# Optimization experiments

Measured on AMD Instinct MI355X. Metric: run time of the kernel, lower is better.

## Reference

```python
import jax, jax.numpy as jnp
import numpy as np

EMBEDDING_DIM = 128
METRIC_MARGIN = 1.0
EPS = 1e-8


def setup_inputs() -> dict:
    key = jax.random.key(0)
    X = jax.random.normal(key, (8192, EMBEDDING_DIM), dtype=jnp.float32)
    return {"X": X}


def reference(X):
    B, d = X.shape
    P = B // 2  # number of positive pairs (2p, 2p+1)
    # Pairwise similarity matrix (original uses broadcasted mul+sum; this is the GEMM form)
    D = (X @ X.T) / d  # [B, B]
    E = jnp.exp(D + METRIC_MARGIN)  # [B, B]

    # For pair p: sum of exp over rows 2p and 2p+1, excluding columns {2p, 2p+1}
    pair_row_sum = E.sum(axis=1).reshape(P, 2).sum(axis=1)  # [P]
    # 2x2 diagonal blocks E[2p:2p+2, 2p:2p+2]
    blocks = jnp.einsum('pipj->pij', E.reshape(P, 2, P, 2))  # [P, 2, 2]
    S = pair_row_sum - blocks.sum(axis=(1, 2))  # [P]

    even = jnp.arange(0, B, 2)
    D_pos = D[even, even + 1]  # D[2p, 2p+1], [P]

    J = jnp.log(EPS + S) - D_pos  # [P]
    loss = jnp.mean(jnp.maximum(J, 0.0) ** 2) / 2.0
    return loss
```

## Files before the change

### kernel.cpp

```cpp
#include <hip/hip_runtime.h>
#include <hip/hip_bf16.h>

#define NROWS 8192
#define DIM   128
#define NPAIR (NROWS / 2)
#define CSPLIT 16
#define COLS_PER_CS (NROWS / CSPLIT)
#define CTILE 64
#define NT (COLS_PER_CS / CTILE)
#define MREP 2
#define ROWS_PER_BLOCK 128

typedef __attribute__((ext_vector_type(8))) short bf16x8;
typedef __attribute__((ext_vector_type(4))) float f32x4;

__device__ inline float exp2_fast(float x) {
#if __has_builtin(__builtin_amdgcn_exp2f)
    return __builtin_amdgcn_exp2f(x);
#else
    return exp2f(x);
#endif
}

__device__ inline unsigned short f2bf(float f) {
    unsigned int u = __float_as_uint(f);
    unsigned int r = (u + 0x7fffu + ((u >> 16) & 1u)) >> 16;
    return (unsigned short)r;
}

#define SCL_F 0.0112710550069450f
#define E1_F  2.7182818284590452f

__global__ __launch_bounds__(256) void k_convert(const float* __restrict__ X,
                                                 unsigned short* __restrict__ Xa,
                                                 unsigned short* __restrict__ Xc) {
    int id = blockIdx.x * 256 + threadIdx.x;
    float4 v = reinterpret_cast<const float4*>(X)[id];
    ushort4 oa, oc;
    oa.x = f2bf(v.x * SCL_F); oa.y = f2bf(v.y * SCL_F);
    oa.z = f2bf(v.z * SCL_F); oa.w = f2bf(v.w * SCL_F);
    oc.x = f2bf(v.x); oc.y = f2bf(v.y); oc.z = f2bf(v.z); oc.w = f2bf(v.w);
    reinterpret_cast<ushort4*>(Xa)[id] = oa;
    reinterpret_cast<ushort4*>(Xc)[id] = oc;
}

__global__ __launch_bounds__(256, 4) void k_rowsum(const unsigned short* __restrict__ Xa,
                                                   const unsigned short* __restrict__ Xc,
                                                   float* __restrict__ partial) {
    __shared__ unsigned short Bt[CTILE * DIM];
    const int tid  = threadIdx.x;
    const int wave = tid >> 6;
    const int lane = tid & 63;
    const int l15  = lane & 15;
    const int lhi  = lane >> 4;
    const int rowbase = blockIdx.x * ROWS_PER_BLOCK + wave * (MREP * 16);
    const int cs = blockIdx.y;

    bf16x8 a00, a01, a02, a03, a10, a11, a12, a13;
    {
        const unsigned short* r0 = Xa + (size_t)(rowbase + l15) * DIM + lhi * 8;
        const unsigned short* r1 = r0 + 16 * DIM;
        a00 = *reinterpret_cast<const bf16x8*>(r0);
        a01 = *reinterpret_cast<const bf16x8*>(r0 + 32);
        a02 = *reinterpret_cast<const bf16x8*>(r0 + 64);
        a03 = *reinterpret_cast<const bf16x8*>(r0 + 96);
        a10 = *reinterpret_cast<const bf16x8*>(r1);
        a11 = *reinterpret_cast<const bf16x8*>(r1 + 32);
        a12 = *reinterpret_cast<const bf16x8*>(r1 + 64);
        a13 = *reinterpret_cast<const bf16x8*>(r1 + 96);
    }
    asm volatile("" : "+v"(a00), "+v"(a01), "+v"(a02), "+v"(a03));
    asm volatile("" : "+v"(a10), "+v"(a11), "+v"(a12), "+v"(a13));

    f32x4 esum0 = {0.f, 0.f, 0.f, 0.f};
    f32x4 esum1 = {0.f, 0.f, 0.f, 0.f};

    const int tcol = tid >> 4;
    const int tseg = tid & 15;
    const unsigned short* gsrc = Xc + (size_t)(cs * COLS_PER_CS + tcol) * DIM + tseg * 8;
    const int lslot = (tcol << 4) | (tseg ^ (tcol & 7));

    bf16x8 st0, st1, st2, st3;
    st0 = *reinterpret_cast<const bf16x8*>(gsrc);
    st1 = *reinterpret_cast<const bf16x8*>(gsrc + 16 * DIM);
    st2 = *reinterpret_cast<const bf16x8*>(gsrc + 32 * DIM);
    st3 = *reinterpret_cast<const bf16x8*>(gsrc + 48 * DIM);

    for (int it = 0; it < NT; ++it) {
        if (it) __syncthreads();
        *reinterpret_cast<bf16x8*>(&Bt[(size_t)(lslot      ) * 8]) = st0;
        *reinterpret_cast<bf16x8*>(&Bt[(size_t)(lslot + 256) * 8]) = st1;
        *reinterpret_cast<bf16x8*>(&Bt[(size_t)(lslot + 512) * 8]) = st2;
        *reinterpret_cast<bf16x8*>(&Bt[(size_t)(lslot + 768) * 8]) = st3;
        __syncthreads();

        if (it + 1 < NT) {
            const unsigned short* nb = gsrc + (size_t)(it + 1) * CTILE * DIM;
            st0 = *reinterpret_cast<const bf16x8*>(nb);
            st1 = *reinterpret_cast<const bf16x8*>(nb + 16 * DIM);
            st2 = *reinterpret_cast<const bf16x8*>(nb + 32 * DIM);
            st3 = *reinterpret_cast<const bf16x8*>(nb + 48 * DIM);
        }

        const int x = l15 & 7;
#pragma unroll
        for (int ct = 0; ct < CTILE / 16; ++ct) {
            const unsigned short* lb = &Bt[(size_t)(ct * 16 + l15) * DIM];
            bf16x8 b0 = *reinterpret_cast<const bf16x8*>(lb + ((lhi      ^ x) * 8));
            bf16x8 b1 = *reinterpret_cast<const bf16x8*>(lb + (((lhi + 4 ) ^ x) * 8));
            bf16x8 b2 = *reinterpret_cast<const bf16x8*>(lb + (((lhi + 8 ) ^ x) * 8));
            bf16x8 b3 = *reinterpret_cast<const bf16x8*>(lb + (((lhi + 12) ^ x) * 8));

            f32x4 d0 = {0.f, 0.f, 0.f, 0.f};
            f32x4 d1 = {0.f, 0.f, 0.f, 0.f};
            d0 = __builtin_amdgcn_mfma_f32_16x16x32_bf16(a00, b0, d0, 0, 0, 0);
            d1 = __builtin_amdgcn_mfma_f32_16x16x32_bf16(a10, b0, d1, 0, 0, 0);
            d0 = __builtin_amdgcn_mfma_f32_16x16x32_bf16(a01, b1, d0, 0, 0, 0);
            d1 = __builtin_amdgcn_mfma_f32_16x16x32_bf16(a11, b1, d1, 0, 0, 0);
            d0 = __builtin_amdgcn_mfma_f32_16x16x32_bf16(a02, b2, d0, 0, 0, 0);
            d1 = __builtin_amdgcn_mfma_f32_16x16x32_bf16(a12, b2, d1, 0, 0, 0);
            d0 = __builtin_amdgcn_mfma_f32_16x16x32_bf16(a03, b3, d0, 0, 0, 0);
            d1 = __builtin_amdgcn_mfma_f32_16x16x32_bf16(a13, b3, d1, 0, 0, 0);

            esum0[0] += exp2_fast(d0[0]); esum0[1] += exp2_fast(d0[1]);
            esum0[2] += exp2_fast(d0[2]); esum0[3] += exp2_fast(d0[3]);
            esum1[0] += exp2_fast(d1[0]); esum1[1] += exp2_fast(d1[1]);
            esum1[2] += exp2_fast(d1[2]); esum1[3] += exp2_fast(d1[3]);
        }
    }

#pragma unroll
    for (int m = 0; m < MREP; ++m) {
#pragma unroll
        for (int j = 0; j < 4; ++j) {
            float v = (m == 0) ? esum0[j] : esum1[j];
            v += __shfl_xor(v, 1, 64);
            v += __shfl_xor(v, 2, 64);
            v += __shfl_xor(v, 4, 64);
            v += __shfl_xor(v, 8, 64);
            if (l15 == 0) {
                int row = rowbase + m * 16 + lhi * 4 + j;
                partial[(size_t)row * CSPLIT + cs] = v * E1_F;
            }
        }
    }
}

__global__ __launch_bounds__(256) void k_loss1(const float* __restrict__ X,
                                               const float* __restrict__ partial,
                                               float* __restrict__ lpart) {
    int p = blockIdx.x * 256 + threadIdx.x;
    const float4* a = reinterpret_cast<const float4*>(X + (size_t)(2 * p) * DIM);
    const float4* b = reinterpret_cast<const float4*>(X + (size_t)(2 * p + 1) * DIM);
    float d00 = 0.f, d01 = 0.f, d11 = 0.f;
#pragma unroll 8
    for (int i = 0; i < DIM / 4; ++i) {
        float4 av = a[i], bv = b[i];
        d00 += av.x * av.x + av.y * av.y + av.z * av.z + av.w * av.w;
        d01 += av.x * bv.x + av.y * bv.y + av.z * bv.z + av.w * bv.w;
        d11 += bv.x * bv.x + bv.y * bv.y + bv.z * bv.z + bv.w * bv.w;
    }
    float D01 = d01 * (1.0f / DIM);
    float blocksum = __expf(d00 * (1.0f / DIM) + 1.0f)
                   + 2.0f * __expf(D01 + 1.0f)
                   + __expf(d11 * (1.0f / DIM) + 1.0f);

    const float4* pp = reinterpret_cast<const float4*>(partial + (size_t)(2 * p) * CSPLIT);
    float S = 0.0f;
#pragma unroll
    for (int i = 0; i < 2 * CSPLIT / 4; ++i) {
        float4 v = pp[i];
        S += v.x + v.y + v.z + v.w;
    }
    S -= blocksum;
    float J = logf(1e-8f + S) - D01;
    float t = fmaxf(J, 0.0f);
    float acc = t * t;

    __shared__ float red[4];
    float v = acc;
#pragma unroll
    for (int off = 32; off >= 1; off >>= 1) v += __shfl_down(v, off, 64);
    if ((threadIdx.x & 63) == 0) red[threadIdx.x >> 6] = v;
    __syncthreads();
    if (threadIdx.x == 0)
        lpart[blockIdx.x] = red[0] + red[1] + red[2] + red[3];
}

__global__ __launch_bounds__(64) void k_final(const float* __restrict__ lpart,
                                              float* __restrict__ out) {
    float v = (threadIdx.x < 16) ? lpart[threadIdx.x] : 0.0f;
#pragma unroll
    for (int off = 8; off >= 1; off >>= 1) v += __shfl_down(v, off, 64);
    if (threadIdx.x == 0) out[0] = v * (1.0f / (2.0f * NPAIR));
}

extern "C" void kernel_launch(void* const* d_in, const int* in_sizes, int n_in,
                              void* d_out, int out_size, void* d_ws, size_t ws_size,
                              hipStream_t stream) {
    const float* X = (const float*)d_in[0];
    float* out = (float*)d_out;

    unsigned short* Xa = (unsigned short*)d_ws;
    unsigned short* Xc = Xa + (size_t)NROWS * DIM;
    float* partial = (float*)(Xc + (size_t)NROWS * DIM);
    float* lpart = partial + (size_t)NROWS * CSPLIT;

    k_convert<<<dim3((NROWS * DIM / 4) / 256), dim3(256), 0, stream>>>(X, Xa, Xc);
    k_rowsum<<<dim3(NROWS / ROWS_PER_BLOCK, CSPLIT), dim3(256), 0, stream>>>(Xa, Xc, partial);
    k_loss1<<<dim3(NPAIR / 256), dim3(256), 0, stream>>>(X, partial, lpart);
    k_final<<<dim3(1), dim3(64), 0, stream>>>(lpart, out);
}
```

Baseline: 41.39 us.

## Double-buffer column tiles via async global-to-LDS loads and enlarge row tile

Replaces register-staged tile loads with direct global-to-LDS async loads into a double-buffered shared tile, so the next tile streams in while the current one is used for MFMA. Each wave now covers 64 rows (MREP 4) instead of 32, doubling the reuse of each LDS tile, and the column split doubles to keep the grid size similar. This raises register pressure from the extra A fragments and accumulators and doubles LDS use. Any downstream code that reads partial with a stride of CSPLIT must now combine 32 partial sums per row.

```diff
diff --git a/kernel.cpp b/kernel.cpp
--- a/kernel.cpp
+++ b/kernel.cpp
@@ -4,12 +4,12 @@
 #define NROWS 8192
 #define DIM   128
 #define NPAIR (NROWS / 2)
-#define CSPLIT 16
+#define CSPLIT 32
 #define COLS_PER_CS (NROWS / CSPLIT)
 #define CTILE 64
 #define NT (COLS_PER_CS / CTILE)
-#define MREP 2
-#define ROWS_PER_BLOCK 128
+#define MREP 4
+#define ROWS_PER_BLOCK 256
 
 typedef __attribute__((ext_vector_type(8))) short bf16x8;
 typedef __attribute__((ext_vector_type(4))) float f32x4;
@@ -27,6 +27,17 @@
     unsigned int r = (u + 0x7fffu + ((u >> 16) & 1u)) >> 16;
     return (unsigned short)r;
 }
+
+#if __has_builtin(__builtin_amdgcn_global_load_lds)
+#define ASYNC16(gp, lp)                                                    \
+    __builtin_amdgcn_global_load_lds(                                      \
+        (const __attribute__((address_space(1))) void*)(gp),               \
+        (__attribute__((address_space(3))) void*)(lp), 16, 0, 0)
+#else
+#define ASYNC16(gp, lp)                                                    \
+    do { *(bf16x8*)((unsigned short*)(lp) + lane * 8) =                    \
+             *(const bf16x8*)(gp); } while (0)
+#endif
 
 #define SCL_F 0.0112710550069450f
 #define E1_F  2.7182818284590452f
@@ -44,10 +55,13 @@
     reinterpret_cast<ushort4*>(Xc)[id] = oc;
 }
 
-__global__ __launch_bounds__(256, 4) void k_rowsum(const unsigned short* __restrict__ Xa,
-                                                   const unsigned short* __restrict__ Xc,
-                                                   float* __restrict__ partial) {
-    __shared__ unsigned short Bt[CTILE * DIM];
+#define MFMA16(A, B, D) __builtin_amdgcn_mfma_f32_16x16x32_bf16(A, B, D, 0, 0, 0)
+
+__global__ __launch_bounds__(256, 4)
+void k_rowsum(const unsigned short* __restrict__ Xa,
+              const unsigned short* __restrict__ Xc,
+              float* __restrict__ partial) {
+    __shared__ unsigned short Bt[2][CTILE * DIM];
     const int tid  = threadIdx.x;
     const int wave = tid >> 6;
     const int lane = tid & 63;
@@ -55,85 +69,96 @@
     const int lhi  = lane >> 4;
     const int rowbase = blockIdx.x * ROWS_PER_BLOCK + wave * (MREP * 16);
     const int cs = blockIdx.y;
+    const int c0 = cs * COLS_PER_CS;
 
     bf16x8 a00, a01, a02, a03, a10, a11, a12, a13;
+    bf16x8 a20, a21, a22, a23, a30, a31, a32, a33;
     {
         const unsigned short* r0 = Xa + (size_t)(rowbase + l15) * DIM + lhi * 8;
         const unsigned short* r1 = r0 + 16 * DIM;
-        a00 = *reinterpret_cast<const bf16x8*>(r0);
-        a01 = *reinterpret_cast<const bf16x8*>(r0 + 32);
-        a02 = *reinterpret_cast<const bf16x8*>(r0 + 64);
-        a03 = *reinterpret_cast<const bf16x8*>(r0 + 96);
-        a10 = *reinterpret_cast<const bf16x8*>(r1);
-        a11 = *reinterpret_cast<const bf16x8*>(r1 + 32);
-        a12 = *reinterpret_cast<const bf16x8*>(r1 + 64);
-        a13 = *reinterpret_cast<const bf16x8*>(r1 + 96);
+        const unsigned short* r2 = r0 + 32 * DIM;
+        const unsigned short* r3 = r0 + 48 * DIM;
+        a00 = *(const bf16x8*)(r0);      a01 = *(const bf16x8*)(r0 + 32);
+        a02 = *(const bf16x8*)(r0 + 64); a03 = *(const bf16x8*)(r0 + 96);
+        a10 = *(const bf16x8*)(r1);      a11 = *(const bf16x8*)(r1 + 32);
+        a12 = *(const bf16x8*)(r1 + 64); a13 = *(const bf16x8*)(r1 + 96);
+        a20 = *(const bf16x8*)(r2);      a21 = *(const bf16x8*)(r2 + 32);
+        a22 = *(const bf16x8*)(r2 + 64); a23 = *(const bf16x8*)(r2 + 96);
+        a30 = *(const bf16x8*)(r3);      a31 = *(const bf16x8*)(r3 + 32);
+        a32 = *(const bf16x8*)(r3 + 64); a33 = *(const bf16x8*)(r3 + 96);
     }
     asm volatile("" : "+v"(a00), "+v"(a01), "+v"(a02), "+v"(a03));
     asm volatile("" : "+v"(a10), "+v"(a11), "+v"(a12), "+v"(a13));
-
-    f32x4 esum0 = {0.f, 0.f, 0.f, 0.f};
-    f32x4 esum1 = {0.f, 0.f, 0.f, 0.f};
-
-    const int tcol = tid >> 4;
-    const int tseg = tid & 15;
-    const unsigned short* gsrc = Xc + (size_t)(cs * COLS_PER_CS + tcol) * DIM + tseg * 8;
-    const int lslot = (tcol << 4) | (tseg ^ (tcol & 7));
-
-    bf16x8 st0, st1, st2, st3;
-    st0 = *reinterpret_cast<const bf16x8*>(gsrc);
-    st1 = *reinterpret_cast<const bf16x8*>(gsrc + 16 * DIM);
-    st2 = *reinterpret_cast<const bf16x8*>(gsrc + 32 * DIM);
-    st3 = *reinterpret_cast<const bf16x8*>(gsrc + 48 * DIM);
-
-    for (int it = 0; it < NT; ++it) {
-        if (it) __syncthreads();
-        *reinterpret_cast<bf16x8*>(&Bt[(size_t)(lslot      ) * 8]) = st0;
-        *reinterpret_cast<bf16x8*>(&Bt[(size_t)(lslot + 256) * 8]) = st1;
-        *reinterpret_cast<bf16x8*>(&Bt[(size_t)(lslot + 512) * 8]) = st2;
-        *reinterpret_cast<bf16x8*>(&Bt[(size_t)(lslot + 768) * 8]) = st3;
+    asm volatile("" : "+v"(a20), "+v"(a21), "+v"(a22), "+v"(a23));
+    asm volatile("" : "+v"(a30), "+v"(a31), "+v"(a32), "+v"(a33));
+
+    f32x4 es0 = {0.f,0.f,0.f,0.f}, es1 = {0.f,0.f,0.f,0.f};
+    f32x4 es2 = {0.f,0.f,0.f,0.f}, es3 = {0.f,0.f,0.f,0.f};
+
+#define STAGE(BUF, TILE)                                                     \
+    do {                                                                     \
+        _Pragma("unroll")                                                    \
+        for (int j = 0; j < 4; ++j) {                                        \
+            int chunk = j * 256 + wave * 64 + lane;                          \
+            int col   = chunk >> 4;                                          \
+            int seg   = chunk & 15;                                          \
+            const unsigned short* g = Xc +                                   \
+                (size_t)(c0 + (TILE) * CTILE + col) * DIM +                  \
+                ((seg ^ (col & 7)) * 8);                                     \
+            ASYNC16(g, &Bt[BUF][(size_t)(j * 256 + wave * 64) * 8]);         \
+        }                                                                    \
+    } while (0)
+
+#define DO_TILE(CUR)                                                         \
+    do {                                                                     \
+        const int x = l15 & 7;                                               \
+        _Pragma("unroll")                                                    \
+        for (int ct = 0; ct < CTILE / 16; ++ct) {                            \
+            const unsigned short* lb = &Bt[CUR][(size_t)(ct * 16 + l15) * DIM]; \
+            bf16x8 b0 = *(const bf16x8*)(lb + (((lhi     ) ^ x) * 8));       \
+            bf16x8 b1 = *(const bf16x8*)(lb + (((lhi +  4) ^ x) * 8));       \
+            bf16x8 b2 = *(const bf16x8*)(lb + (((lhi +  8) ^ x) * 8));       \
+            bf16x8 b3 = *(const bf16x8*)(lb + (((lhi + 12) ^ x) * 8));       \
+            f32x4 d0 = {0.f,0.f,0.f,0.f}, d1 = {0.f,0.f,0.f,0.f};            \
+            f32x4 d2 = {0.f,0.f,0.f,0.f}, d3 = {0.f,0.f,0.f,0.f};            \
+            d0 = MFMA16(a00, b0, d0); d1 = MFMA16(a10, b0, d1);              \
+            d2 = MFMA16(a20, b0, d2); d3 = MFMA16(a30, b0, d3);              \
+            d0 = MFMA16(a01, b1, d0); d1 = MFMA16(a11, b1, d1);              \
+            d2 = MFMA16(a21, b1, d2); d3 = MFMA16(a31, b1, d3);              \
+            d0 = MFMA16(a02, b2, d0); d1 = MFMA16(a12, b2, d1);              \
+            d2 = MFMA16(a22, b2, d2); d3 = MFMA16(a32, b2, d3);              \
+            d0 = MFMA16(a03, b3, d0); d1 = MFMA16(a13, b3, d1);              \
+            d2 = MFMA16(a23, b3, d2); d3 = MFMA16(a33, b3, d3);              \
+            es0[0] += exp2_fast(d0[0]); es0[1] += exp2_fast(d0[1]);          \
+            es0[2] += exp2_fast(d0[2]); es0[3] += exp2_fast(d0[3]);          \
+            es1[0] += exp2_fast(d1[0]); es1[1] += exp2_fast(d1[1]);          \
+            es1[2] += exp2_fast(d1[2]); es1[3] += exp2_fast(d1[3]);          \
+            es2[0] += exp2_fast(d2[0]); es2[1] += exp2_fast(d2[1]);          \
+            es2[2] += exp2_fast(d2[2]); es2[3] += exp2_fast(d2[3]);          \
+            es3[0] += exp2_fast(d3[0]); es3[1] += exp2_fast(d3[1]);          \
+            es3[2] += exp2_fast(d3[2]); es3[3] += exp2_fast(d3[3]);          \
+        }                                                                    \
+    } while (0)
+
+    STAGE(0, 0);
+    asm volatile("s_waitcnt vmcnt(0)" ::: "memory");
+    __syncthreads();
+
+    int cur = 0;
+    for (int t = 0; t < NT; ++t) {
+        if (t + 1 < NT) STAGE(cur ^ 1, t + 1);
+        DO_TILE(cur);
+        asm volatile("s_waitcnt vmcnt(0)" ::: "memory");
         __syncthreads();
-
-        if (it + 1 < NT) {
-            const unsigned short* nb = gsrc + (size_t)(it + 1) * CTILE * DIM;
-            st0 = *reinterpret_cast<const bf16x8*>(nb);
-            st1 = *reinterpret_cast<const bf16x8*>(nb + 16 * DIM);
-            st2 = *reinterpret_cast<const bf16x8*>(nb + 32 * DIM);
-            st3 = *reinterpret_cast<const bf16x8*>(nb + 48 * DIM);
-        }
-
-        const int x = l15 & 7;
-#pragma unroll
-        for (int ct = 0; ct < CTILE / 16; ++ct) {
-            const unsigned short* lb = &Bt[(size_t)(ct * 16 + l15) * DIM];
-            bf16x8 b0 = *reinterpret_cast<const bf16x8*>(lb + ((lhi      ^ x) * 8));
-            bf16x8 b1 = *reinterpret_cast<const bf16x8*>(lb + (((lhi + 4 ) ^ x) * 8));
-            bf16x8 b2 = *reinterpret_cast<const bf16x8*>(lb + (((lhi + 8 ) ^ x) * 8));
-            bf16x8 b3 = *reinterpret_cast<const bf16x8*>(lb + (((lhi + 12) ^ x) * 8));
-
-            f32x4 d0 = {0.f, 0.f, 0.f, 0.f};
-            f32x4 d1 = {0.f, 0.f, 0.f, 0.f};
-            d0 = __builtin_amdgcn_mfma_f32_16x16x32_bf16(a00, b0, d0, 0, 0, 0);
-            d1 = __builtin_amdgcn_mfma_f32_16x16x32_bf16(a10, b0, d1, 0, 0, 0);
-            d0 = __builtin_amdgcn_mfma_f32_16x16x32_bf16(a01, b1, d0, 0, 0, 0);
-            d1 = __builtin_amdgcn_mfma_f32_16x16x32_bf16(a11, b1, d1, 0, 0, 0);
-            d0 = __builtin_amdgcn_mfma_f32_16x16x32_bf16(a02, b2, d0, 0, 0, 0);
-            d1 = __builtin_amdgcn_mfma_f32_16x16x32_bf16(a12, b2, d1, 0, 0, 0);
-            d0 = __builtin_amdgcn_mfma_f32_16x16x32_bf16(a03, b3, d0, 0, 0, 0);
-            d1 = __builtin_amdgcn_mfma_f32_16x16x32_bf16(a13, b3, d1, 0, 0, 0);
-
-            esum0[0] += exp2_fast(d0[0]); esum0[1] += exp2_fast(d0[1]);
-            esum0[2] += exp2_fast(d0[2]); esum0[3] += exp2_fast(d0[3]);
-            esum1[0] += exp2_fast(d1[0]); esum1[1] += exp2_fast(d1[1]);
-            esum1[2] += exp2_fast(d1[2]); esum1[3] += exp2_fast(d1[3]);
-        }
+        cur ^= 1;
     }
 
 #pragma unroll
     for (int m = 0; m < MREP; ++m) {
 #pragma unroll
         for (int j = 0; j < 4; ++j) {
-            float v = (m == 0) ? esum0[j] : esum1[j];
+            float v = (m == 0) ? es0[j] : (m == 1) ? es1[j]
+                    : (m == 2) ? es2[j] : es3[j];
             v += __shfl_xor(v, 1, 64);
             v += __shfl_xor(v, 2, 64);
             v += __shfl_xor(v, 4, 64);
```

Result: slower. 142.6 us (+244.5%).

## Exploit Gram-matrix symmetry: compute upper-triangle tiles, emit row and column sums

Applied to the files above, without the earlier changes.

The row-sum kernel is replaced by one that launches a 64x64 grid of 128x128 tiles. Blocks below the diagonal exit immediately, so each off-diagonal tile is computed once. Each computed tile yields its row sums and, through a shared-memory column accumulator, the column sums for the mirrored tile. This roughly halves the MFMA and exp2 work. The cost is extra shuffles, shared-memory reductions and a second barrier per block, and each block now does only one tile with no pipelined B loads. It also relies on the scaled-A times unscaled-C product being close to symmetric.

```diff
diff --git a/kernel.cpp b/kernel.cpp
--- a/kernel.cpp
+++ b/kernel.cpp
@@ -4,12 +4,11 @@
 #define NROWS 8192
 #define DIM   128
 #define NPAIR (NROWS / 2)
-#define CSPLIT 16
-#define COLS_PER_CS (NROWS / CSPLIT)
-#define CTILE 64
-#define NT (COLS_PER_CS / CTILE)
-#define MREP 2
-#define ROWS_PER_BLOCK 128
+#define NB    64
+#define BROWS 128
+#define CSPLIT 64
+#define MREP  2
+#define NCT   (BROWS / 16)
 
 typedef __attribute__((ext_vector_type(8))) short bf16x8;
 typedef __attribute__((ext_vector_type(4))) float f32x4;
@@ -44,104 +43,113 @@
     reinterpret_cast<ushort4*>(Xc)[id] = oc;
 }
 
-__global__ __launch_bounds__(256, 4) void k_rowsum(const unsigned short* __restrict__ Xa,
-                                                   const unsigned short* __restrict__ Xc,
-                                                   float* __restrict__ partial) {
-    __shared__ unsigned short Bt[CTILE * DIM];
+#define MFMA16(A, B, D) __builtin_amdgcn_mfma_f32_16x16x32_bf16(A, B, D, 0, 0, 0)
+
+__global__ __launch_bounds__(256, 4)
+void k_pairsum(const unsigned short* __restrict__ Xa,
+               const unsigned short* __restrict__ Xc,
+               float* __restrict__ partial) {
+    const int bi = blockIdx.x;
+    const int bj = blockIdx.y;
+    if (bj < bi) return;
+
+    __shared__ unsigned short Bt[BROWS * DIM];
+    __shared__ float colacc[4][BROWS];
     const int tid  = threadIdx.x;
     const int wave = tid >> 6;
     const int lane = tid & 63;
     const int l15  = lane & 15;
     const int lhi  = lane >> 4;
-    const int rowbase = blockIdx.x * ROWS_PER_BLOCK + wave * (MREP * 16);
-    const int cs = blockIdx.y;
+    const int rowbase = bi * BROWS + wave * (MREP * 16);
+
+    {
+        const int tcol = tid >> 4, tseg = tid & 15;
+        const int lslot = (tcol << 4) | (tseg ^ (tcol & 7));
+        const unsigned short* g = Xc + (size_t)(bj * BROWS + tcol) * DIM + tseg * 8;
+        bf16x8 s0 = *(const bf16x8*)(g);
+        bf16x8 s1 = *(const bf16x8*)(g + 16 * DIM);
+        bf16x8 s2 = *(const bf16x8*)(g + 32 * DIM);
+        bf16x8 s3 = *(const bf16x8*)(g + 48 * DIM);
+        *(bf16x8*)&Bt[(size_t)(lslot       ) * 8] = s0;
+        *(bf16x8*)&Bt[(size_t)(lslot + 256 ) * 8] = s1;
+        *(bf16x8*)&Bt[(size_t)(lslot + 512 ) * 8] = s2;
+        *(bf16x8*)&Bt[(size_t)(lslot + 768 ) * 8] = s3;
+        s0 = *(const bf16x8*)(g + 64 * DIM);
+        s1 = *(const bf16x8*)(g + 80 * DIM);
+        s2 = *(const bf16x8*)(g + 96 * DIM);
+        s3 = *(const bf16x8*)(g + 112 * DIM);
+        *(bf16x8*)&Bt[(size_t)(lslot + 1024) * 8] = s0;
+        *(bf16x8*)&Bt[(size_t)(lslot + 1280) * 8] = s1;
+        *(bf16x8*)&Bt[(size_t)(lslot + 1536) * 8] = s2;
+        *(bf16x8*)&Bt[(size_t)(lslot + 1792) * 8] = s3;
+    }
 
     bf16x8 a00, a01, a02, a03, a10, a11, a12, a13;
     {
         const unsigned short* r0 = Xa + (size_t)(rowbase + l15) * DIM + lhi * 8;
         const unsigned short* r1 = r0 + 16 * DIM;
-        a00 = *reinterpret_cast<const bf16x8*>(r0);
-        a01 = *reinterpret_cast<const bf16x8*>(r0 + 32);
-        a02 = *reinterpret_cast<const bf16x8*>(r0 + 64);
-        a03 = *reinterpret_cast<const bf16x8*>(r0 + 96);
-        a10 = *reinterpret_cast<const bf16x8*>(r1);
-        a11 = *reinterpret_cast<const bf16x8*>(r1 + 32);
-        a12 = *reinterpret_cast<const bf16x8*>(r1 + 64);
-        a13 = *reinterpret_cast<const bf16x8*>(r1 + 96);
+        a00 = *(const bf16x8*)(r0);      a01 = *(const bf16x8*)(r0 + 32);
+        a02 = *(const bf16x8*)(r0 + 64); a03 = *(const bf16x8*)(r0 + 96);
+        a10 = *(const bf16x8*)(r1);      a11 = *(const bf16x8*)(r1 + 32);
+        a12 = *(const bf16x8*)(r1 + 64); a13 = *(const bf16x8*)(r1 + 96);
     }
     asm volatile("" : "+v"(a00), "+v"(a01), "+v"(a02), "+v"(a03));
     asm volatile("" : "+v"(a10), "+v"(a11), "+v"(a12), "+v"(a13));
 
-    f32x4 esum0 = {0.f, 0.f, 0.f, 0.f};
-    f32x4 esum1 = {0.f, 0.f, 0.f, 0.f};
-
-    const int tcol = tid >> 4;
-    const int tseg = tid & 15;
-    const unsigned short* gsrc = Xc + (size_t)(cs * COLS_PER_CS + tcol) * DIM + tseg * 8;
-    const int lslot = (tcol << 4) | (tseg ^ (tcol & 7));
-
-    bf16x8 st0, st1, st2, st3;
-    st0 = *reinterpret_cast<const bf16x8*>(gsrc);
-    st1 = *reinterpret_cast<const bf16x8*>(gsrc + 16 * DIM);
-    st2 = *reinterpret_cast<const bf16x8*>(gsrc + 32 * DIM);
-    st3 = *reinterpret_cast<const bf16x8*>(gsrc + 48 * DIM);
-
-    for (int it = 0; it < NT; ++it) {
-        if (it) __syncthreads();
-        *reinterpret_cast<bf16x8*>(&Bt[(size_t)(lslot      ) * 8]) = st0;
-        *reinterpret_cast<bf16x8*>(&Bt[(size_t)(lslot + 256) * 8]) = st1;
-        *reinterpret_cast<bf16x8*>(&Bt[(size_t)(lslot + 512) * 8]) = st2;
-        *reinterpret_cast<bf16x8*>(&Bt[(size_t)(lslot + 768) * 8]) = st3;
-        __syncthreads();
-
-        if (it + 1 < NT) {
-            const unsigned short* nb = gsrc + (size_t)(it + 1) * CTILE * DIM;
-            st0 = *reinterpret_cast<const bf16x8*>(nb);
-            st1 = *reinterpret_cast<const bf16x8*>(nb + 16 * DIM);
-            st2 = *reinterpret_cast<const bf16x8*>(nb + 32 * DIM);
-            st3 = *reinterpret_cast<const bf16x8*>(nb + 48 * DIM);
-        }
-
-        const int x = l15 & 7;
-#pragma unroll
-        for (int ct = 0; ct < CTILE / 16; ++ct) {
-            const unsigned short* lb = &Bt[(size_t)(ct * 16 + l15) * DIM];
-            bf16x8 b0 = *reinterpret_cast<const bf16x8*>(lb + ((lhi      ^ x) * 8));
-            bf16x8 b1 = *reinterpret_cast<const bf16x8*>(lb + (((lhi + 4 ) ^ x) * 8));
-            bf16x8 b2 = *reinterpret_cast<const bf16x8*>(lb + (((lhi + 8 ) ^ x) * 8));
-            bf16x8 b3 = *reinterpret_cast<const bf16x8*>(lb + (((lhi + 12) ^ x) * 8));
-
-            f32x4 d0 = {0.f, 0.f, 0.f, 0.f};
-            f32x4 d1 = {0.f, 0.f, 0.f, 0.f};
-            d0 = __builtin_amdgcn_mfma_f32_16x16x32_bf16(a00, b0, d0, 0, 0, 0);
-            d1 = __builtin_amdgcn_mfma_f32_16x16x32_bf16(a10, b0, d1, 0, 0, 0);
-            d0 = __builtin_amdgcn_mfma_f32_16x16x32_bf16(a01, b1, d0, 0, 0, 0);
-            d1 = __builtin_amdgcn_mfma_f32_16x16x32_bf16(a11, b1, d1, 0, 0, 0);
-            d0 = __builtin_amdgcn_mfma_f32_16x16x32_bf16(a02, b2, d0, 0, 0, 0);
-            d1 = __builtin_amdgcn_mfma_f32_16x16x32_bf16(a12, b2, d1, 0, 0, 0);
-            d0 = __builtin_amdgcn_mfma_f32_16x16x32_bf16(a03, b3, d0, 0, 0, 0);
-            d1 = __builtin_amdgcn_mfma_f32_16x16x32_bf16(a13, b3, d1, 0, 0, 0);
-
-            esum0[0] += exp2_fast(d0[0]); esum0[1] += exp2_fast(d0[1]);
-            esum0[2] += exp2_fast(d0[2]); esum0[3] += exp2_fast(d0[3]);
-            esum1[0] += exp2_fast(d1[0]); esum1[1] += exp2_fast(d1[1]);
-            esum1[2] += exp2_fast(d1[2]); esum1[3] += exp2_fast(d1[3]);
-        }
+    f32x4 es0 = {0.f,0.f,0.f,0.f}, es1 = {0.f,0.f,0.f,0.f};
+
+    __syncthreads();
+
+    const int x = l15 & 7;
+#pragma unroll 2
+    for (int ct = 0; ct < NCT; ++ct) {
+        const unsigned short* lb = &Bt[(size_t)(ct * 16 + l15) * DIM];
+        bf16x8 b0 = *(const bf16x8*)(lb + (((lhi     ) ^ x) * 8));
+        bf16x8 b1 = *(const bf16x8*)(lb + (((lhi +  4) ^ x) * 8));
+        bf16x8 b2 = *(const bf16x8*)(lb + (((lhi +  8) ^ x) * 8));
+        bf16x8 b3 = *(const bf16x8*)(lb + (((lhi + 12) ^ x) * 8));
+
+        f32x4 d0 = {0.f,0.f,0.f,0.f}, d1 = {0.f,0.f,0.f,0.f};
+        d0 = MFMA16(a00, b0, d0); d1 = MFMA16(a10, b0, d1);
+        d0 = MFMA16(a01, b1, d0); d1 = MFMA16(a11, b1, d1);
+        d0 = MFMA16(a02, b2, d0); d1 = MFMA16(a12, b2, d1);
+        d0 = MFMA16(a03, b3, d0); d1 = MFMA16(a13, b3, d1);
+
+        float e0 = exp2_fast(d0[0]), e1 = exp2_fast(d0[1]);
+        float e2 = exp2_fast(d0[2]), e3 = exp2_fast(d0[3]);
+        float e4 = exp2_fast(d1[0]), e5 = exp2_fast(d1[1]);
+        float e6 = exp2_fast(d1[2]), e7 = exp2_fast(d1[3]);
+        es0[0] += e0; es0[1] += e1; es0[2] += e2; es0[3] += e3;
+        es1[0] += e4; es1[1] += e5; es1[2] += e6; es1[3] += e7;
+
+        float cs = ((e0 + e1) + (e2 + e3)) + ((e4 + e5) + (e6 + e7));
+        cs += __shfl_xor(cs, 16, 64);
+        cs += __shfl_xor(cs, 32, 64);
+        if (lhi == 0) colacc[wave][ct * 16 + l15] = cs;
     }
 
 #pragma unroll
     for (int m = 0; m < MREP; ++m) {
 #pragma unroll
         for (int j = 0; j < 4; ++j) {
-            float v = (m == 0) ? esum0[j] : esum1[j];
+            float v = (m == 0) ? es0[j] : es1[j];
             v += __shfl_xor(v, 1, 64);
             v += __shfl_xor(v, 2, 64);
             v += __shfl_xor(v, 4, 64);
             v += __shfl_xor(v, 8, 64);
             if (l15 == 0) {
                 int row = rowbase + m * 16 + lhi * 4 + j;
-                partial[(size_t)row * CSPLIT + cs] = v * E1_F;
+                partial[(size_t)row * CSPLIT + bj] = v * E1_F;
             }
+        }
+    }
+
+    if (bi != bj) {
+        __syncthreads();
+        if (tid < BROWS) {
+            float v = colacc[0][tid] + colacc[1][tid]
+                    + colacc[2][tid] + colacc[3][tid];
+            partial[(size_t)(bj * BROWS + tid) * CSPLIT + bi] = v * E1_F;
         }
     }
 }
@@ -207,7 +215,7 @@
     float* lpart = partial + (size_t)NROWS * CSPLIT;
 
     k_convert<<<dim3((NROWS * DIM / 4) / 256), dim3(256), 0, stream>>>(X, Xa, Xc);
-    k_rowsum<<<dim3(NROWS / ROWS_PER_BLOCK, CSPLIT), dim3(256), 0, stream>>>(Xa, Xc, partial);
+    k_pairsum<<<dim3(NB, NB), dim3(256), 0, stream>>>(Xa, Xc, partial);
     k_loss1<<<dim3(NPAIR / 256), dim3(256), 0, stream>>>(X, partial, lpart);
     k_final<<<dim3(1), dim3(64), 0, stream>>>(lpart, out);
 }
```

Measured after the change: 50.19 us. 1.21x slower.
